# Optimization experiments

Hardware: AMD Instinct MI355X
Metric: run time of the kernel (lower is better)

The kernel has to match this reference:

```python
import jax, jax.numpy as jnp
import numpy as np

HIDDEN_DIM = 64
MAX_DISP = 48
NUM_GROUPS = 8


def setup_inputs() -> dict:
    key = jax.random.key(0)
    k1, k2 = jax.random.split(key)
    n, c, h, w = 4, HIDDEN_DIM, 160, 320
    return {
        "l_fmap": jax.random.normal(k1, (n, c, h, w), dtype=jnp.float32),
        "r_fmap": jax.random.normal(k2, (n, c, h, w), dtype=jnp.float32),
    }


def _cost_volume(l_fmap, r_fmap, max_disp, num_groups):
    n, c, h, w = l_fmap.shape
    cg = c // num_groups
    l5 = l_fmap.reshape(n, num_groups, cg, h, w)
    # Pre-pad right fmap on the left so each disparity shift is a static-size slice.
    r_pad = jnp.pad(r_fmap, ((0, 0), (0, 0), (0, 0), (max_disp - 1, 0)))
    col = jnp.arange(w)
    one = jnp.asarray(1.0, l_fmap.dtype)

    def step(d):
        # r shifted right by d pixels (right-image feature aligned to left at disparity d)
        r_sh = jax.lax.dynamic_slice(r_pad, (0, 0, 0, max_disp - 1 - d), (n, c, h, w))
        r5 = r_sh.reshape(n, num_groups, cg, h, w)
        cost = jnp.mean(l5 * r5, axis=2)  # [n, G, h, w] group-wise correlation
        # Columns < d are out of range; original leaves them at the init value 1.0.
        return jnp.where(col >= d, cost, one)

    vol = jax.lax.map(step, jnp.arange(max_disp))  # [D, n, G, h, w]
    return jnp.transpose(vol, (1, 2, 0, 3, 4))  # [n, G, D, h, w]


def reference(l_fmap, r_fmap):
    return _cost_volume(l_fmap, r_fmap, MAX_DISP, NUM_GROUPS)
```

## Files before the change

kernel.cpp:

```cpp
#include <hip/hip_runtime.h>

#define N_  4
#define C_  64
#define H_  160
#define W_  320
#define G_  8
#define CG_ 8
#define D_  48

#define ROWS_PER_BLK 4
#define TPB (ROWS_PER_BLK * (W_ / 4))
#define HW_ (H_ * W_)
#define SWZW 336

__device__ __forceinline__ int swz_idx(int w) { return w + (w >> 5); }

__global__ __launch_bounds__(TPB) void gcv_kernel(
    const float* __restrict__ l, const float* __restrict__ r,
    float* __restrict__ out) {
  const int n   = blockIdx.z;
  const int g   = blockIdx.y;
  const int hb  = blockIdx.x;
  const int tid = threadIdx.x;
  const int row = tid / 80;
  const int col = tid % 80;
  const int w0  = col * 4;
  const int h   = hb * ROWS_PER_BLK + row;

  __shared__ float r_lds[ROWS_PER_BLK * CG_ * SWZW];

  const int in_base = ((n * C_ + g * CG_) * H_ + h) * W_ + w0;
  const float* lp = l + in_base;
  const float* rp = r + in_base;

  float lv[4][8];
  float slot[4][8];

  const int sb = w0 + (w0 >> 5);
  float* myrow = &r_lds[(row * CG_) * SWZW];

  #pragma unroll
  for (int k = 0; k < 8; ++k) {
    const float4 lq = *reinterpret_cast<const float4*>(lp + k * HW_);
    lv[0][k] = lq.x; lv[1][k] = lq.y; lv[2][k] = lq.z; lv[3][k] = lq.w;
    const float4 rq = *reinterpret_cast<const float4*>(rp + k * HW_);
    slot[0][k] = rq.x; slot[1][k] = rq.y; slot[2][k] = rq.z; slot[3][k] = rq.w;
    float* lr = myrow + k * SWZW;
    lr[sb + 0] = rq.x; lr[sb + 1] = rq.y; lr[sb + 2] = rq.z; lr[sb + 3] = rq.w;
  }
  __syncthreads();

  float* op = out + ((n * G_ + g) * D_ * H_ + h) * W_ + w0;

  for (int d4 = 0; d4 < D_; d4 += 4) {
    #pragma unroll
    for (int p = 0; p < 4; ++p) {
      const int d = d4 + p;
      float o[4];
      #pragma unroll
      for (int j = 0; j < 4; ++j) {
        float acc = 0.0f;
        #pragma unroll
        for (int k = 0; k < 8; ++k)
          acc += lv[j][k] * slot[(j - p + 4) & 3][k];
        o[j] = (w0 + j >= d) ? acc * 0.125f : 1.0f;
      }
      *reinterpret_cast<float4*>(op + d * HW_) =
          make_float4(o[0], o[1], o[2], o[3]);
      int widx = w0 - d - 1;
      int cw = widx < 0 ? 0 : widx;
      int a = cw + (cw >> 5);
      #pragma unroll
      for (int k = 0; k < 8; ++k)
        slot[(3 - p) & 3][k] = myrow[k * SWZW + a];
    }
  }
}

extern "C" void kernel_launch(void* const* d_in, const int* in_sizes, int n_in,
                              void* d_out, int out_size, void* d_ws, size_t ws_size,
                              hipStream_t stream) {
  const float* l = (const float*)d_in[0];
  const float* r = (const float*)d_in[1];
  float* out = (float*)d_out;
  dim3 grid(H_ / ROWS_PER_BLK, G_, N_);
  dim3 block(TPB);
  hipLaunchKernelGGL(gcv_kernel, grid, block, 0, stream, l, r, out);
}
```

Baseline: 392.0 us.

## Replace scalar swizzled LDS reads with aligned float4 double-buffered window loads

Drops the swizzled shared-memory layout and stores the right feature rows unpadded, so each thread writes and reads them with aligned float4 accesses. Instead of one scalar LDS read per channel per disparity, each group of four disparities now loads a full 4-wide window per channel into one of two ping-pong register buffers (X/Y). The disparity loop is fully unrolled so the buffer selection resolves at compile time. This cuts LDS instruction count and index arithmetic, at the cost of more registers and larger code; the removed swizzle may reintroduce bank conflicts.

```diff
diff --git a/kernel.cpp b/kernel.cpp
--- a/kernel.cpp
+++ b/kernel.cpp
@@ -11,9 +11,7 @@
 #define ROWS_PER_BLK 4
 #define TPB (ROWS_PER_BLK * (W_ / 4))
 #define HW_ (H_ * W_)
-#define SWZW 336
 
-__device__ __forceinline__ int swz_idx(int w) { return w + (w >> 5); }
 
 __global__ __launch_bounds__(TPB) void gcv_kernel(
     const float* __restrict__ l, const float* __restrict__ r,
@@ -27,52 +25,70 @@
   const int w0  = col * 4;
   const int h   = hb * ROWS_PER_BLK + row;
 
-  __shared__ float r_lds[ROWS_PER_BLK * CG_ * SWZW];
+  __shared__ float r_lds[ROWS_PER_BLK * CG_ * W_];
 
   const int in_base = ((n * C_ + g * CG_) * H_ + h) * W_ + w0;
   const float* lp = l + in_base;
   const float* rp = r + in_base;
 
   float lv[4][8];
-  float slot[4][8];
+  float X[8][4], Y[8][4];
 
-  const int sb = w0 + (w0 >> 5);
-  float* myrow = &r_lds[(row * CG_) * SWZW];
+  float* myrow = &r_lds[row * CG_ * W_];
 
   #pragma unroll
   for (int k = 0; k < 8; ++k) {
     const float4 lq = *reinterpret_cast<const float4*>(lp + k * HW_);
     lv[0][k] = lq.x; lv[1][k] = lq.y; lv[2][k] = lq.z; lv[3][k] = lq.w;
     const float4 rq = *reinterpret_cast<const float4*>(rp + k * HW_);
-    slot[0][k] = rq.x; slot[1][k] = rq.y; slot[2][k] = rq.z; slot[3][k] = rq.w;
-    float* lr = myrow + k * SWZW;
-    lr[sb + 0] = rq.x; lr[sb + 1] = rq.y; lr[sb + 2] = rq.z; lr[sb + 3] = rq.w;
+    X[k][0] = rq.x; X[k][1] = rq.y; X[k][2] = rq.z; X[k][3] = rq.w;
+    *reinterpret_cast<float4*>(&myrow[k * W_ + w0]) = rq;
   }
   __syncthreads();
 
+  {
+    int cb = w0 - 4; if (cb < 0) cb = 0;
+    #pragma unroll
+    for (int k = 0; k < 8; ++k) {
+      const float4 v = *reinterpret_cast<const float4*>(&myrow[k * W_ + cb]);
+      Y[k][0] = v.x; Y[k][1] = v.y; Y[k][2] = v.z; Y[k][3] = v.w;
+    }
+  }
+
   float* op = out + ((n * G_ + g) * D_ * H_ + h) * W_ + w0;
 
-  for (int d4 = 0; d4 < D_; d4 += 4) {
+  #pragma unroll
+  for (int t = 0; t < D_ / 4; ++t) {
+    const int d4 = 4 * t;
+    float (&H)[8][4] = (t & 1) ? Y : X;
+    float (&L)[8][4] = (t & 1) ? X : Y;
+
     #pragma unroll
     for (int p = 0; p < 4; ++p) {
       const int d = d4 + p;
       float o[4];
       #pragma unroll
       for (int j = 0; j < 4; ++j) {
+        const int off = 4 + j - p;
         float acc = 0.0f;
         #pragma unroll
-        for (int k = 0; k < 8; ++k)
-          acc += lv[j][k] * slot[(j - p + 4) & 3][k];
+        for (int k = 0; k < 8; ++k) {
+          const float rv = (off >= 4) ? H[k][off - 4] : L[k][off];
+          acc += lv[j][k] * rv;
+        }
         o[j] = (w0 + j >= d) ? acc * 0.125f : 1.0f;
       }
       *reinterpret_cast<float4*>(op + d * HW_) =
           make_float4(o[0], o[1], o[2], o[3]);
-      int widx = w0 - d - 1;
-      int cw = widx < 0 ? 0 : widx;
-      int a = cw + (cw >> 5);
+    }
+
+    if (t < D_ / 4 - 1) {
+      int cb = w0 - d4 - 8; if (cb < 0) cb = 0;
       #pragma unroll
-      for (int k = 0; k < 8; ++k)
-        slot[(3 - p) & 3][k] = myrow[k * SWZW + a];
+      for (int k = 0; k < 8; ++k) {
+        const float4 v = *reinterpret_cast<const float4*>(&myrow[k * W_ + cb]);
+        H[k][0] = v.x; H[k][1] = v.y; H[k][2] = v.z; H[k][3] = v.w;
+      }
     }
   }
 }
```

Result: faster. 380.6 us (-2.9%).
